# Kernel optimization log

Measured on AMD Instinct MI355X. Metric: run time of the kernel, lower is better.

## Reference

```python
import jax, jax.numpy as jnp
import numpy as np

N = 50000          # nodes
E = 1_600_000      # edges (before self-loops)
F_IN = 256
HID = 32
HEADS = 4
OUT = 64
NEG_SLOPE = 0.2


def setup_inputs() -> dict:
    key = jax.random.key(0)
    ks = jax.random.split(key, 10)
    x = jax.random.normal(ks[0], (N, F_IN), dtype=jnp.float32)
    edge_index = jax.random.randint(ks[1], (2, E), 0, N, dtype=jnp.int64)
    # layer 1: input_dim -> hidden*heads
    W1 = jax.random.normal(ks[2], (F_IN, HEADS * HID), dtype=jnp.float32) / np.sqrt(F_IN)
    att_src1 = jax.random.normal(ks[3], (HEADS, HID), dtype=jnp.float32) / np.sqrt(HID)
    att_dst1 = jax.random.normal(ks[4], (HEADS, HID), dtype=jnp.float32) / np.sqrt(HID)
    b1 = jnp.zeros((HEADS * HID,), dtype=jnp.float32)
    # layer 2: hidden*heads -> out, 1 head, concat=False
    W2 = jax.random.normal(ks[5], (HEADS * HID, OUT), dtype=jnp.float32) / np.sqrt(HEADS * HID)
    att_src2 = jax.random.normal(ks[6], (1, OUT), dtype=jnp.float32) / np.sqrt(OUT)
    att_dst2 = jax.random.normal(ks[7], (1, OUT), dtype=jnp.float32) / np.sqrt(OUT)
    b2 = jnp.zeros((OUT,), dtype=jnp.float32)
    return {"x": x, "edge_index": edge_index, "W1": W1, "att_src1": att_src1,
            "att_dst1": att_dst1, "b1": b1, "W2": W2, "att_src2": att_src2,
            "att_dst2": att_dst2, "b2": b2}


def gat_layer(x, src, dst, W, a_src, a_dst, bias, heads, out_dim, concat):
    n = x.shape[0]
    h = (x @ W).reshape(n, heads, out_dim)              # [N,H,C]
    # per-node attention logits
    al_src = jnp.sum(h * a_src[None], axis=-1)          # [N,H]
    al_dst = jnp.sum(h * a_dst[None], axis=-1)          # [N,H]
    e = al_src[src] + al_dst[dst]                       # [E',H]
    e = jax.nn.leaky_relu(e, NEG_SLOPE)
    # segment softmax over incoming edges of each dst node
    emax = jax.ops.segment_max(e, dst, num_segments=n)  # [N,H]
    ee = jnp.exp(e - emax[dst])
    denom = jax.ops.segment_sum(ee, dst, num_segments=n)
    alpha = ee / denom[dst]                             # [E',H]
    msg = h[src] * alpha[:, :, None]                    # [E',H,C]
    out = jax.ops.segment_sum(msg, dst, num_segments=n)  # [N,H,C]
    if concat:
        out = out.reshape(n, heads * out_dim)
    else:
        out = out.mean(axis=1)
    return out + bias


def reference(x, edge_index, W1, att_src1, att_dst1, b1, W2, att_src2, att_dst2, b2):
    # add self-loops (PyG GATConv default)
    loop = jnp.arange(N, dtype=edge_index.dtype)
    src = jnp.concatenate([edge_index[0], loop])
    dst = jnp.concatenate([edge_index[1], loop])
    # eval mode: dropout(p=0.5) is identity
    h = gat_layer(x, src, dst, W1, att_src1, att_dst1, b1, HEADS, HID, True)
    h = jax.nn.elu(h)
    out = gat_layer(h, src, dst, W2, att_src2, att_dst2, b2, 1, OUT, False)
    return out
```

## Files before the change

kernel.cpp:

```cpp
#include <hip/hip_runtime.h>
#include <hip/hip_bf16.h>
#include <hip/hip_fp16.h>
#include <math.h>

#define NNODES 50000
#define NEDGES 1600000
#define ETOT   (NEDGES + NNODES)
#define F_INN  256
#define NEG_SLOPE 0.2f
#define NBUCK  782
#define BCAP   2624
#define CNBLK  256
#define CBT    1024

__global__ __launch_bounds__(128) void detect_kernel(const unsigned int* __restrict__ ei,
                                                     int* __restrict__ flag) {
    __shared__ int nz;
    if (threadIdx.x == 0) nz = 0;
    __syncthreads();
    unsigned int v = ei[2 * threadIdx.x + 1];
    if (v != 0u) nz = 1;
    __syncthreads();
    if (threadIdx.x == 0) *flag = nz;
}

__device__ __forceinline__ void load_edge(const void* ei, bool is32, int i, int& s, int& d) {
    if (i < NEDGES) {
        if (is32) {
            const int* p = (const int*)ei;
            s = p[i]; d = p[NEDGES + i];
        } else {
            const long long* p = (const long long*)ei;
            s = (int)p[i]; d = (int)p[NEDGES + i];
        }
    } else {
        s = i - NEDGES; d = s;
    }
}

__global__ __launch_bounds__(CBT) void convert_kernel(const void* __restrict__ ei,
                                                      const int* __restrict__ flag,
                                                      int* __restrict__ bcnt,
                                                      int2* __restrict__ bpair) {
    __shared__ int hist[NBUCK];
    __shared__ int base[NBUCK];
    const int t = threadIdx.x;
    const int chunk = (ETOT + CNBLK - 1) / CNBLK;
    const int i0 = blockIdx.x * chunk;
    const int i1 = min(i0 + chunk, ETOT);
    for (int k = t; k < NBUCK; k += CBT) hist[k] = 0;
    __syncthreads();
    const bool is32 = (*flag) != 0;
    for (int i = i0 + t; i < i1; i += CBT) {
        int s, d; load_edge(ei, is32, i, s, d);
        atomicAdd(&hist[d >> 6], 1);
    }
    __syncthreads();
    for (int k = t; k < NBUCK; k += CBT) {
        int c = hist[k];
        base[k] = c ? atomicAdd(&bcnt[k], c) : 0;
        hist[k] = 0;
    }
    __syncthreads();
    for (int i = i0 + t; i < i1; i += CBT) {
        int s, d; load_edge(ei, is32, i, s, d);
        int b = d >> 6;
        int pos = base[b] + atomicAdd(&hist[b], 1);
        bpair[(size_t)b * BCAP + pos] = make_int2(s, d);
    }
}

__global__ __launch_bounds__(1024) void bucket_scan_kernel(const int* __restrict__ bcnt,
                                                           int* __restrict__ bbase,
                                                           int* __restrict__ rowptr) {
    __shared__ int wsum[16];
    const int t = threadIdx.x, lane = t & 63, wid = t >> 6;
    int v = (t < NBUCK) ? bcnt[t] : 0;
    int incl = v;
    #pragma unroll
    for (int off = 1; off < 64; off <<= 1) {
        int u = __shfl_up(incl, off);
        if (lane >= off) incl += u;
    }
    if (lane == 63) wsum[wid] = incl;
    __syncthreads();
    if (wid == 0) {
        int wv = (lane < 16) ? wsum[lane] : 0;
        #pragma unroll
        for (int off = 1; off < 16; off <<= 1) {
            int u = __shfl_up(wv, off);
            if (lane >= off) wv += u;
        }
        if (lane < 16) wsum[lane] = wv;
    }
    __syncthreads();
    int base = (wid == 0) ? 0 : wsum[wid - 1];
    if (t < NBUCK) bbase[t] = base + incl - v;
    if (t == 0) rowptr[NNODES] = ETOT;
}

__global__ __launch_bounds__(256) void bscatter_kernel(const int2* __restrict__ bpair,
                                                       const int* __restrict__ bcnt,
                                                       const int* __restrict__ bbase,
                                                       int* __restrict__ rowptr,
                                                       int* __restrict__ ssrc) {
    __shared__ int cnt[64];
    __shared__ int s_widx[64];
    const int b = blockIdx.x;
    const int t = threadIdx.x;
    if (t < 64) cnt[t] = 0;
    __syncthreads();
    const int n = bcnt[b];
    const int2* bp = bpair + (size_t)b * BCAP;
    for (int i = t; i < n; i += 256) atomicAdd(&cnt[bp[i].y & 63], 1);
    __syncthreads();
    if (t < 64) {
        int v = cnt[t];
        int incl = v;
        #pragma unroll
        for (int off = 1; off < 64; off <<= 1) {
            int u = __shfl_up(incl, off);
            if (t >= off) incl += u;
        }
        int excl = bbase[b] + incl - v;
        int node = (b << 6) + t;
        if (node < NNODES) rowptr[node] = excl;
        s_widx[t] = excl;
    }
    __syncthreads();
    for (int i = t; i < n; i += 256) {
        int2 e = bp[i];
        int pos = atomicAdd(&s_widx[e.y & 63], 1);
        ssrc[pos] = e.x;
    }
}

__global__ __launch_bounds__(256) void gemm1_kernel(const float* __restrict__ x,
                                                    const float* __restrict__ W,
                                                    const float* __restrict__ atts,
                                                    const float* __restrict__ attd,
                                                    __half2* __restrict__ h1h,
                                                    float* __restrict__ als,
                                                    float* __restrict__ ald) {
    __shared__ float xs[32][68];
    __shared__ float ws[32][128];
    const int tid = threadIdx.x;
    const int tx = tid & 15, ty = tid >> 4;
    const int row0 = blockIdx.x * 64;
    float acc[4][8];
    #pragma unroll
    for (int r = 0; r < 4; ++r)
        #pragma unroll
        for (int c = 0; c < 8; ++c) acc[r][c] = 0.f;

    const int lr = tid >> 2;
    const int lk = (tid & 3) * 8;
    const int wk = tid >> 3;
    const int wc = (tid & 7) * 16;

    for (int k0 = 0; k0 < F_INN; k0 += 32) {
        float4 v0 = make_float4(0.f,0.f,0.f,0.f), v1 = v0;
        int gr = row0 + lr;
        if (gr < NNODES) {
            const float* xp = x + (size_t)gr * F_INN + k0 + lk;
            v0 = *(const float4*)xp; v1 = *(const float4*)(xp + 4);
        }
        xs[lk+0][lr]=v0.x; xs[lk+1][lr]=v0.y; xs[lk+2][lr]=v0.z; xs[lk+3][lr]=v0.w;
        xs[lk+4][lr]=v1.x; xs[lk+5][lr]=v1.y; xs[lk+6][lr]=v1.z; xs[lk+7][lr]=v1.w;
        const float* wp = W + (size_t)(k0 + wk) * 128 + wc;
        #pragma unroll
        for (int q = 0; q < 4; ++q)
            *(float4*)&ws[wk][wc + q*4] = *(const float4*)(wp + q*4);
        __syncthreads();
        #pragma unroll
        for (int k = 0; k < 32; ++k) {
            float4 av = *(const float4*)&xs[k][ty*4];
            float4 b0 = *(const float4*)&ws[k][tx*8];
            float4 b1 = *(const float4*)&ws[k][tx*8+4];
            const float a_[4] = {av.x,av.y,av.z,av.w};
            const float b_[8] = {b0.x,b0.y,b0.z,b0.w,b1.x,b1.y,b1.z,b1.w};
            #pragma unroll
            for (int r = 0; r < 4; ++r)
                #pragma unroll
                for (int c = 0; c < 8; ++c)
                    acc[r][c] = fmaf(a_[r], b_[c], acc[r][c]);
        }
        __syncthreads();
    }
    #pragma unroll
    for (int r = 0; r < 4; ++r) {
        int gr = row0 + ty*4 + r;
        bool valid = gr < NNODES;
        float ps = 0.f, pd = 0.f;
        if (valid) {
            float4 pack;
            __half2* pk = (__half2*)&pack;
            pk[0] = __floats2half2_rn(acc[r][0], acc[r][1]);
            pk[1] = __floats2half2_rn(acc[r][2], acc[r][3]);
            pk[2] = __floats2half2_rn(acc[r][4], acc[r][5]);
            pk[3] = __floats2half2_rn(acc[r][6], acc[r][7]);
            *(float4*)(h1h + (size_t)gr*64 + tx*4) = pack;
            #pragma unroll
            for (int c = 0; c < 8; ++c) {
                ps = fmaf(acc[r][c], atts[tx*8 + c], ps);
                pd = fmaf(acc[r][c], attd[tx*8 + c], pd);
            }
        }
        ps += __shfl_xor(ps, 1); ps += __shfl_xor(ps, 2);
        pd += __shfl_xor(pd, 1); pd += __shfl_xor(pd, 2);
        if (valid && (tx & 3) == 0) {
            int hd = tx >> 2;
            als[gr*4 + hd] = ps;
            ald[gr*4 + hd] = pd;
        }
    }
}

__global__ __launch_bounds__(256) void gemm2_kernel(const float* __restrict__ x2,
                                                    const float* __restrict__ W,
                                                    const float* __restrict__ atts,
                                                    const float* __restrict__ attd,
                                                    float* __restrict__ h2,
                                                    float* __restrict__ als,
                                                    float* __restrict__ ald) {
    __shared__ float xs[32][68];
    __shared__ float ws[32][64];
    const int tid = threadIdx.x;
    const int tx = tid & 15, ty = tid >> 4;
    const int row0 = blockIdx.x * 64;
    float acc[4][4];
    #pragma unroll
    for (int r = 0; r < 4; ++r)
        #pragma unroll
        for (int c = 0; c < 4; ++c) acc[r][c] = 0.f;

    const int lr = tid >> 2;
    const int lk = (tid & 3) * 8;
    const int wk = tid >> 3;
    const int wc = (tid & 7) * 8;

    for (int k0 = 0; k0 < 128; k0 += 32) {
        float4 v0 = make_float4(0.f,0.f,0.f,0.f), v1 = v0;
        int gr = row0 + lr;
        if (gr < NNODES) {
            const float* xp = x2 + (size_t)gr * 128 + k0 + lk;
            v0 = *(const float4*)xp; v1 = *(const float4*)(xp + 4);
        }
        xs[lk+0][lr]=v0.x; xs[lk+1][lr]=v0.y; xs[lk+2][lr]=v0.z; xs[lk+3][lr]=v0.w;
        xs[lk+4][lr]=v1.x; xs[lk+5][lr]=v1.y; xs[lk+6][lr]=v1.z; xs[lk+7][lr]=v1.w;
        const float* wp = W + (size_t)(k0 + wk) * 64 + wc;
        *(float4*)&ws[wk][wc]     = *(const float4*)wp;
        *(float4*)&ws[wk][wc + 4] = *(const float4*)(wp + 4);
        __syncthreads();
        #pragma unroll
        for (int k = 0; k < 32; ++k) {
            float4 av = *(const float4*)&xs[k][ty*4];
            float4 bv = *(const float4*)&ws[k][tx*4];
            const float a_[4] = {av.x,av.y,av.z,av.w};
            const float b_[4] = {bv.x,bv.y,bv.z,bv.w};
            #pragma unroll
            for (int r = 0; r < 4; ++r)
                #pragma unroll
                for (int c = 0; c < 4; ++c)
                    acc[r][c] = fmaf(a_[r], b_[c], acc[r][c]);
        }
        __syncthreads();
    }
    #pragma unroll
    for (int r = 0; r < 4; ++r) {
        int gr = row0 + ty*4 + r;
        bool valid = gr < NNODES;
        float ps = 0.f, pd = 0.f;
        if (valid) {
            *(float4*)&h2[(size_t)gr*64 + tx*4] = make_float4(acc[r][0],acc[r][1],acc[r][2],acc[r][3]);
            #pragma unroll
            for (int c = 0; c < 4; ++c) {
                ps = fmaf(acc[r][c], atts[tx*4 + c], ps);
                pd = fmaf(acc[r][c], attd[tx*4 + c], pd);
            }
        }
        ps += __shfl_xor(ps, 1); ps += __shfl_xor(ps, 2);
        ps += __shfl_xor(ps, 4); ps += __shfl_xor(ps, 8);
        pd += __shfl_xor(pd, 1); pd += __shfl_xor(pd, 2);
        pd += __shfl_xor(pd, 4); pd += __shfl_xor(pd, 8);
        if (valid && tx == 0) {
            als[gr] = ps;
            ald[gr] = pd;
        }
    }
}

__device__ __forceinline__ float lrelu(float e) { return e > 0.f ? e : NEG_SLOPE * e; }

__global__ __launch_bounds__(256) void edge1_kernel(const int* __restrict__ rowptr,
                                                    const int* __restrict__ ssrc,
                                                    const float* __restrict__ als,
                                                    const float* __restrict__ ald,
                                                    const __half2* __restrict__ h1h,
                                                    const float* __restrict__ b1,
                                                    float* __restrict__ x2) {
    __shared__ float s_alpha[4][256];
    __shared__ int   s_sidx[4][64];
    __shared__ int   s_nch[4];
    const int lane = threadIdx.x & 63;
    const int wid  = threadIdx.x >> 6;
    const int d = blockIdx.x * 4 + wid;
    const int start = rowptr[d], end = rowptr[d + 1];
    const int deg = end - start;
    float4 aldv = *(const float4*)&ald[d * 4];

    float l0=0.f, l1=0.f, l2=0.f, l3=0.f;
    float4 ex0 = make_float4(0,0,0,0), ex1 = ex0;
    int ss0 = 0, ss1 = 0;
    int it = 0;
    for (int j = start + lane; j < end; j += 64, ++it) {
        int s = ssrc[j];
        float4 a = *(const float4*)&als[s * 4];
        float e0 = __expf(lrelu(a.x + aldv.x));
        float e1 = __expf(lrelu(a.y + aldv.y));
        float e2 = __expf(lrelu(a.z + aldv.z));
        float e3 = __expf(lrelu(a.w + aldv.w));
        if (it == 0)      { ex0 = make_float4(e0,e1,e2,e3); ss0 = s; }
        else if (it == 1) { ex1 = make_float4(e0,e1,e2,e3); ss1 = s; }
        l0 += e0; l1 += e1; l2 += e2; l3 += e3;
    }
    #pragma unroll
    for (int off = 32; off >= 1; off >>= 1) {
        l0 += __shfl_xor(l0, off); l1 += __shfl_xor(l1, off);
        l2 += __shfl_xor(l2, off); l3 += __shfl_xor(l3, off);
    }
    float il0 = 1.f/l0, il1 = 1.f/l1, il2 = 1.f/l2, il3 = 1.f/l3;

    const int nch = (deg + 63) >> 6;
    if (lane == 0) s_nch[wid] = nch;
    __syncthreads();
    const int maxch = max(max(s_nch[0], s_nch[1]), max(s_nch[2], s_nch[3]));

    const int h = lane >> 4;
    float s0 = 0.f, s1 = 0.f;
    for (int c = 0; c < maxch; ++c) {
        const int base = start + c * 64;
        if (c < nch) {
            int j = base + lane;
            if (j < end) {
                int s; float4 ex;
                if (c == 0)      { s = ss0; ex = ex0; }
                else if (c == 1) { s = ss1; ex = ex1; }
                else {
                    s = ssrc[j];
                    float4 a = *(const float4*)&als[s * 4];
                    ex = make_float4(__expf(lrelu(a.x + aldv.x)),
                                     __expf(lrelu(a.y + aldv.y)),
                                     __expf(lrelu(a.z + aldv.z)),
                                     __expf(lrelu(a.w + aldv.w)));
                }
                s_sidx[wid][lane] = s;
                float4 al = make_float4(ex.x*il0, ex.y*il1, ex.z*il2, ex.w*il3);
                *(float4*)&s_alpha[wid][lane * 4] = al;
            }
        }
        __syncthreads();
        if (c < nch) {
            const int cnt = min(64, end - base);
            int jj = 0;
            for (; jj + 3 < cnt; jj += 4) {
                int sA = __builtin_amdgcn_readfirstlane(s_sidx[wid][jj]);
                int sB = __builtin_amdgcn_readfirstlane(s_sidx[wid][jj + 1]);
                int sC = __builtin_amdgcn_readfirstlane(s_sidx[wid][jj + 2]);
                int sD = __builtin_amdgcn_readfirstlane(s_sidx[wid][jj + 3]);
                float aA = s_alpha[wid][jj*4 + h];
                float aB = s_alpha[wid][jj*4 + 4 + h];
                float aC = s_alpha[wid][jj*4 + 8 + h];
                float aD = s_alpha[wid][jj*4 + 12 + h];
                float2 hA = __half22float2(h1h[(size_t)sA * 64 + lane]);
                float2 hB = __half22float2(h1h[(size_t)sB * 64 + lane]);
                float2 hC = __half22float2(h1h[(size_t)sC * 64 + lane]);
                float2 hD = __half22float2(h1h[(size_t)sD * 64 + lane]);
                s0 = fmaf(hA.x, aA, s0); s1 = fmaf(hA.y, aA, s1);
                s0 = fmaf(hB.x, aB, s0); s1 = fmaf(hB.y, aB, s1);
                s0 = fmaf(hC.x, aC, s0); s1 = fmaf(hC.y, aC, s1);
                s0 = fmaf(hD.x, aD, s0); s1 = fmaf(hD.y, aD, s1);
            }
            for (; jj < cnt; ++jj) {
                int sA = __builtin_amdgcn_readfirstlane(s_sidx[wid][jj]);
                float aA = s_alpha[wid][jj*4 + h];
                float2 hA = __half22float2(h1h[(size_t)sA * 64 + lane]);
                s0 = fmaf(hA.x, aA, s0); s1 = fmaf(hA.y, aA, s1);
            }
        }
        __syncthreads();
    }
    const int col = lane << 1;
    float o0 = s0 + b1[col], o1 = s1 + b1[col + 1];
    o0 = o0 > 0.f ? o0 : expm1f(o0);
    o1 = o1 > 0.f ? o1 : expm1f(o1);
    *(float2*)&x2[(size_t)d * 128 + col] = make_float2(o0, o1);
}

__global__ __launch_bounds__(256) void edge2_kernel(const int* __restrict__ rowptr,
                                                    const int* __restrict__ ssrc,
                                                    const float* __restrict__ als,
                                                    const float* __restrict__ ald,
                                                    const float* __restrict__ h2,
                                                    const float* __restrict__ b2,
                                                    float* __restrict__ out) {
    __shared__ float s_alpha[4][64];
    __shared__ int   s_sidx[4][64];
    __shared__ int   s_nch[4];
    const int lane = threadIdx.x & 63;
    const int wid  = threadIdx.x >> 6;
    const int d = blockIdx.x * 4 + wid;
    const int start = rowptr[d], end = rowptr[d + 1];
    const int deg = end - start;
    float aldd = ald[d];

    float l = 0.f;
    float ex0 = 0.f, ex1 = 0.f;
    int ss0 = 0, ss1 = 0;
    int it = 0;
    for (int j = start + lane; j < end; j += 64, ++it) {
        int s = ssrc[j];
        float e = __expf(lrelu(als[s] + aldd));
        if (it == 0)      { ex0 = e; ss0 = s; }
        else if (it == 1) { ex1 = e; ss1 = s; }
        l += e;
    }
    #pragma unroll
    for (int off = 32; off >= 1; off >>= 1) l += __shfl_xor(l, off);
    float invl = 1.f / l;

    const int nch = (deg + 63) >> 6;
    if (lane == 0) s_nch[wid] = nch;
    __syncthreads();
    const int maxch = max(max(s_nch[0], s_nch[1]), max(s_nch[2], s_nch[3]));

    float acc = 0.f;
    for (int c = 0; c < maxch; ++c) {
        const int base = start + c * 64;
        if (c < nch) {
            int j = base + lane;
            if (j < end) {
                int s; float e;
                if (c == 0)      { s = ss0; e = ex0; }
                else if (c == 1) { s = ss1; e = ex1; }
                else { s = ssrc[j]; e = __expf(lrelu(als[s] + aldd)); }
                s_sidx[wid][lane] = s;
                s_alpha[wid][lane] = e * invl;
            }
        }
        __syncthreads();
        if (c < nch) {
            const int cnt = min(64, end - base);
            int jj = 0;
            for (; jj + 3 < cnt; jj += 4) {
                int sA = __builtin_amdgcn_readfirstlane(s_sidx[wid][jj]);
                int sB = __builtin_amdgcn_readfirstlane(s_sidx[wid][jj + 1]);
                int sC = __builtin_amdgcn_readfirstlane(s_sidx[wid][jj + 2]);
                int sD = __builtin_amdgcn_readfirstlane(s_sidx[wid][jj + 3]);
                float aA = s_alpha[wid][jj],     aB = s_alpha[wid][jj + 1];
                float aC = s_alpha[wid][jj + 2], aD = s_alpha[wid][jj + 3];
                float hA = h2[(size_t)sA * 64 + lane];
                float hB = h2[(size_t)sB * 64 + lane];
                float hC = h2[(size_t)sC * 64 + lane];
                float hD = h2[(size_t)sD * 64 + lane];
                acc = fmaf(hA, aA, acc);
                acc = fmaf(hB, aB, acc);
                acc = fmaf(hC, aC, acc);
                acc = fmaf(hD, aD, acc);
            }
            for (; jj < cnt; ++jj) {
                int sA = __builtin_amdgcn_readfirstlane(s_sidx[wid][jj]);
                float aA = s_alpha[wid][jj];
                acc = fmaf(h2[(size_t)sA * 64 + lane], aA, acc);
            }
        }
        __syncthreads();
    }
    out[(size_t)d * 64 + lane] = acc + b2[lane];
}

extern "C" void kernel_launch(void* const* d_in, const int* in_sizes, int n_in,
                              void* d_out, int out_size, void* d_ws, size_t ws_size,
                              hipStream_t stream) {
    const float* x   = (const float*)d_in[0];
    const void*  ei  = d_in[1];
    const float* W1  = (const float*)d_in[2];
    const float* as1 = (const float*)d_in[3];
    const float* ad1 = (const float*)d_in[4];
    const float* b1  = (const float*)d_in[5];
    const float* W2  = (const float*)d_in[6];
    const float* as2 = (const float*)d_in[7];
    const float* ad2 = (const float*)d_in[8];
    const float* b2  = (const float*)d_in[9];
    float* out = (float*)d_out;

    char* p = (char*)d_ws;
    auto alloc = [&](size_t bytes) {
        char* r = p;
        p += (bytes + 255) & ~(size_t)255;
        return r;
    };
    int2*     bpair  = (int2*)alloc(sizeof(int2) * (size_t)NBUCK * BCAP);
    int*      bcnt   = (int*)alloc(sizeof(int) * NBUCK);
    int*      bbase  = (int*)alloc(sizeof(int) * NBUCK);
    int*      ssrc   = (int*)alloc(sizeof(int) * ETOT);
    int*      rowptr = (int*)alloc(sizeof(int) * (NNODES + 1));
    int*      flag   = (int*)alloc(256);
    float*    als1   = (float*)alloc(sizeof(float) * NNODES * 4);
    float*    ald1   = (float*)alloc(sizeof(float) * NNODES * 4);
    float*    als2v  = (float*)alloc(sizeof(float) * NNODES);
    float*    ald2v  = (float*)alloc(sizeof(float) * NNODES);
    __half2*  h1h    = (__half2*)alloc(sizeof(__half2) * NNODES * 64);
    float*    x2     = (float*)alloc(sizeof(float) * NNODES * 128);
    float*    h2     = (float*)alloc(sizeof(float) * NNODES * 64);

    hipMemsetAsync(bcnt, 0, sizeof(int) * NBUCK, stream);

    detect_kernel<<<1, 128, 0, stream>>>((const unsigned int*)ei, flag);
    convert_kernel<<<CNBLK, CBT, 0, stream>>>(ei, flag, bcnt, bpair);
    bucket_scan_kernel<<<1, 1024, 0, stream>>>(bcnt, bbase, rowptr);
    bscatter_kernel<<<NBUCK, 256, 0, stream>>>(bpair, bcnt, bbase, rowptr, ssrc);
    gemm1_kernel<<<(NNODES + 63) / 64, 256, 0, stream>>>(x, W1, as1, ad1, h1h, als1, ald1);
    edge1_kernel<<<(NNODES + 3) / 4, 256, 0, stream>>>(rowptr, ssrc, als1, ald1, h1h, b1, x2);
    gemm2_kernel<<<(NNODES + 63) / 64, 256, 0, stream>>>(x2, W2, as2, ad2, h2, als2v, ald2v);
    edge2_kernel<<<(NNODES + 3) / 4, 256, 0, stream>>>(rowptr, ssrc, als2v, ald2v, h2, b2, out);
}
```

Measured before the change: 343.6 us.

## Double-buffer shared tiles with register prefetch and XOR swizzle in both GEMMs

Both projection GEMMs now prefetch the next K-slice of x and W into registers while computing on the current shared-memory buffer, then store it into a second buffer. This leaves one barrier per iteration instead of two and overlaps global load latency with FMAs. The transposed x tile also uses an XOR swizzle on the column index to reduce LDS bank conflicts on the scattered stores, and the W tile gets padding. The cost is double the shared memory per block and more live registers, which may lower occupancy.

```diff
diff --git a/kernel.cpp b/kernel.cpp
--- a/kernel.cpp
+++ b/kernel.cpp
@@ -142,8 +142,8 @@
                                                     __half2* __restrict__ h1h,
                                                     float* __restrict__ als,
                                                     float* __restrict__ ald) {
-    __shared__ float xs[32][68];
-    __shared__ float ws[32][128];
+    __shared__ float xs[2][32][68];
+    __shared__ float ws[2][32][132];
     const int tid = threadIdx.x;
     const int tx = tid & 15, ty = tid >> 4;
     const int row0 = blockIdx.x * 64;
@@ -155,28 +155,47 @@
 
     const int lr = tid >> 2;
     const int lk = (tid & 3) * 8;
+    const int sw = (lk & 8) << 1;
+    const int cl = lr ^ sw;
     const int wk = tid >> 3;
     const int wc = (tid & 7) * 16;
 
-    for (int k0 = 0; k0 < F_INN; k0 += 32) {
-        float4 v0 = make_float4(0.f,0.f,0.f,0.f), v1 = v0;
-        int gr = row0 + lr;
-        if (gr < NNODES) {
-            const float* xp = x + (size_t)gr * F_INN + k0 + lk;
-            v0 = *(const float4*)xp; v1 = *(const float4*)(xp + 4);
-        }
-        xs[lk+0][lr]=v0.x; xs[lk+1][lr]=v0.y; xs[lk+2][lr]=v0.z; xs[lk+3][lr]=v0.w;
-        xs[lk+4][lr]=v1.x; xs[lk+5][lr]=v1.y; xs[lk+6][lr]=v1.z; xs[lk+7][lr]=v1.w;
-        const float* wp = W + (size_t)(k0 + wk) * 128 + wc;
-        #pragma unroll
-        for (int q = 0; q < 4; ++q)
-            *(float4*)&ws[wk][wc + q*4] = *(const float4*)(wp + q*4);
-        __syncthreads();
+    const int gr = row0 + lr;
+    const bool gok = gr < NNODES;
+    const float* xpb = x + (size_t)gr * F_INN + lk;
+    const float* wpb = W + (size_t)wk * 128 + wc;
+
+    float4 rx0 = make_float4(0,0,0,0), rx1 = rx0;
+    float4 rw0, rw1, rw2, rw3;
+    if (gok) { rx0 = *(const float4*)xpb; rx1 = *(const float4*)(xpb + 4); }
+    rw0 = *(const float4*)(wpb);      rw1 = *(const float4*)(wpb + 4);
+    rw2 = *(const float4*)(wpb + 8);  rw3 = *(const float4*)(wpb + 12);
+    xs[0][lk+0][cl]=rx0.x; xs[0][lk+1][cl]=rx0.y; xs[0][lk+2][cl]=rx0.z; xs[0][lk+3][cl]=rx0.w;
+    xs[0][lk+4][cl]=rx1.x; xs[0][lk+5][cl]=rx1.y; xs[0][lk+6][cl]=rx1.z; xs[0][lk+7][cl]=rx1.w;
+    *(float4*)&ws[0][wk][wc]      = rw0;
+    *(float4*)&ws[0][wk][wc + 4]  = rw1;
+    *(float4*)&ws[0][wk][wc + 8]  = rw2;
+    *(float4*)&ws[0][wk][wc + 12] = rw3;
+    __syncthreads();
+
+    for (int k0 = 0; k0 < 8; ++k0) {
+        const int cur = k0 & 1;
+        const bool more = (k0 < 7);
+        if (more) {
+            const int kk = (k0 + 1) * 32;
+            if (gok) {
+                const float* xp = xpb + kk;
+                rx0 = *(const float4*)xp; rx1 = *(const float4*)(xp + 4);
+            }
+            const float* wp = wpb + (size_t)kk * 128;
+            rw0 = *(const float4*)(wp);      rw1 = *(const float4*)(wp + 4);
+            rw2 = *(const float4*)(wp + 8);  rw3 = *(const float4*)(wp + 12);
+        }
         #pragma unroll
         for (int k = 0; k < 32; ++k) {
-            float4 av = *(const float4*)&xs[k][ty*4];
-            float4 b0 = *(const float4*)&ws[k][tx*8];
-            float4 b1 = *(const float4*)&ws[k][tx*8+4];
+            float4 av = *(const float4*)&xs[cur][k][(ty*4) ^ ((k & 8) << 1)];
+            float4 b0 = *(const float4*)&ws[cur][k][tx*8];
+            float4 b1 = *(const float4*)&ws[cur][k][tx*8+4];
             const float a_[4] = {av.x,av.y,av.z,av.w};
             const float b_[8] = {b0.x,b0.y,b0.z,b0.w,b1.x,b1.y,b1.z,b1.w};
             #pragma unroll
@@ -185,12 +204,22 @@
                 for (int c = 0; c < 8; ++c)
                     acc[r][c] = fmaf(a_[r], b_[c], acc[r][c]);
         }
+        if (more) {
+            const int nb = cur ^ 1;
+            xs[nb][lk+0][cl]=rx0.x; xs[nb][lk+1][cl]=rx0.y; xs[nb][lk+2][cl]=rx0.z; xs[nb][lk+3][cl]=rx0.w;
+            xs[nb][lk+4][cl]=rx1.x; xs[nb][lk+5][cl]=rx1.y; xs[nb][lk+6][cl]=rx1.z; xs[nb][lk+7][cl]=rx1.w;
+            *(float4*)&ws[nb][wk][wc]      = rw0;
+            *(float4*)&ws[nb][wk][wc + 4]  = rw1;
+            *(float4*)&ws[nb][wk][wc + 8]  = rw2;
+            *(float4*)&ws[nb][wk][wc + 12] = rw3;
+        }
         __syncthreads();
     }
+
     #pragma unroll
     for (int r = 0; r < 4; ++r) {
-        int gr = row0 + ty*4 + r;
-        bool valid = gr < NNODES;
+        int gor = row0 + ty*4 + r;
+        bool valid = gor < NNODES;
         float ps = 0.f, pd = 0.f;
         if (valid) {
             float4 pack;
@@ -199,7 +228,7 @@
             pk[1] = __floats2half2_rn(acc[r][2], acc[r][3]);
             pk[2] = __floats2half2_rn(acc[r][4], acc[r][5]);
             pk[3] = __floats2half2_rn(acc[r][6], acc[r][7]);
-            *(float4*)(h1h + (size_t)gr*64 + tx*4) = pack;
+            *(float4*)(h1h + (size_t)gor*64 + tx*4) = pack;
             #pragma unroll
             for (int c = 0; c < 8; ++c) {
                 ps = fmaf(acc[r][c], atts[tx*8 + c], ps);
@@ -210,8 +239,8 @@
         pd += __shfl_xor(pd, 1); pd += __shfl_xor(pd, 2);
         if (valid && (tx & 3) == 0) {
             int hd = tx >> 2;
-            als[gr*4 + hd] = ps;
-            ald[gr*4 + hd] = pd;
+            als[gor*4 + hd] = ps;
+            ald[gor*4 + hd] = pd;
         }
     }
 }
@@ -223,8 +252,8 @@
                                                     float* __restrict__ h2,
                                                     float* __restrict__ als,
                                                     float* __restrict__ ald) {
-    __shared__ float xs[32][68];
-    __shared__ float ws[32][64];
+    __shared__ float xs[2][32][68];
+    __shared__ float ws[2][32][68];
     const int tid = threadIdx.x;
     const int tx = tid & 15, ty = tid >> 4;
     const int row0 = blockIdx.x * 64;
@@ -236,26 +265,42 @@
 
     const int lr = tid >> 2;
     const int lk = (tid & 3) * 8;
+    const int sw = (lk & 8) << 1;
+    const int cl = lr ^ sw;
     const int wk = tid >> 3;
     const int wc = (tid & 7) * 8;
 
-    for (int k0 = 0; k0 < 128; k0 += 32) {
-        float4 v0 = make_float4(0.f,0.f,0.f,0.f), v1 = v0;
-        int gr = row0 + lr;
-        if (gr < NNODES) {
-            const float* xp = x2 + (size_t)gr * 128 + k0 + lk;
-            v0 = *(const float4*)xp; v1 = *(const float4*)(xp + 4);
-        }
-        xs[lk+0][lr]=v0.x; xs[lk+1][lr]=v0.y; xs[lk+2][lr]=v0.z; xs[lk+3][lr]=v0.w;
-        xs[lk+4][lr]=v1.x; xs[lk+5][lr]=v1.y; xs[lk+6][lr]=v1.z; xs[lk+7][lr]=v1.w;
-        const float* wp = W + (size_t)(k0 + wk) * 64 + wc;
-        *(float4*)&ws[wk][wc]     = *(const float4*)wp;
-        *(float4*)&ws[wk][wc + 4] = *(const float4*)(wp + 4);
-        __syncthreads();
+    const int gr = row0 + lr;
+    const bool gok = gr < NNODES;
+    const float* xpb = x2 + (size_t)gr * 128 + lk;
+    const float* wpb = W + (size_t)wk * 64 + wc;
+
+    float4 rx0 = make_float4(0,0,0,0), rx1 = rx0;
+    float4 rw0, rw1;
+    if (gok) { rx0 = *(const float4*)xpb; rx1 = *(const float4*)(xpb + 4); }
+    rw0 = *(const float4*)(wpb); rw1 = *(const float4*)(wpb + 4);
+    xs[0][lk+0][cl]=rx0.x; xs[0][lk+1][cl]=rx0.y; xs[0][lk+2][cl]=rx0.z; xs[0][lk+3][cl]=rx0.w;
+    xs[0][lk+4][cl]=rx1.x; xs[0][lk+5][cl]=rx1.y; xs[0][lk+6][cl]=rx1.z; xs[0][lk+7][cl]=rx1.w;
+    *(float4*)&ws[0][wk][wc]     = rw0;
+    *(float4*)&ws[0][wk][wc + 4] = rw1;
+    __syncthreads();
+
+    for (int k0 = 0; k0 < 4; ++k0) {
+        const int cur = k0 & 1;
+        const bool more = (k0 < 3);
+        if (more) {
+            const int kk = (k0 + 1) * 32;
+            if (gok) {
+                const float* xp = xpb + kk;
+                rx0 = *(const float4*)xp; rx1 = *(const float4*)(xp + 4);
+            }
+            const float* wp = wpb + (size_t)kk * 64;
+            rw0 = *(const float4*)(wp); rw1 = *(const float4*)(wp + 4);
+        }
         #pragma unroll
         for (int k = 0; k < 32; ++k) {
-            float4 av = *(const float4*)&xs[k][ty*4];
-            float4 bv = *(const float4*)&ws[k][tx*4];
+            float4 av = *(const float4*)&xs[cur][k][(ty*4) ^ ((k & 8) << 1)];
+            float4 bv = *(const float4*)&ws[cur][k][tx*4];
             const float a_[4] = {av.x,av.y,av.z,av.w};
             const float b_[4] = {bv.x,bv.y,bv.z,bv.w};
             #pragma unroll
@@ -264,15 +309,23 @@
                 for (int c = 0; c < 4; ++c)
                     acc[r][c] = fmaf(a_[r], b_[c], acc[r][c]);
         }
+        if (more) {
+            const int nb = cur ^ 1;
+            xs[nb][lk+0][cl]=rx0.x; xs[nb][lk+1][cl]=rx0.y; xs[nb][lk+2][cl]=rx0.z; xs[nb][lk+3][cl]=rx0.w;
+            xs[nb][lk+4][cl]=rx1.x; xs[nb][lk+5][cl]=rx1.y; xs[nb][lk+6][cl]=rx1.z; xs[nb][lk+7][cl]=rx1.w;
+            *(float4*)&ws[nb][wk][wc]     = rw0;
+            *(float4*)&ws[nb][wk][wc + 4] = rw1;
+        }
         __syncthreads();
     }
+
     #pragma unroll
     for (int r = 0; r < 4; ++r) {
-        int gr = row0 + ty*4 + r;
-        bool valid = gr < NNODES;
+        int gor = row0 + ty*4 + r;
+        bool valid = gor < NNODES;
         float ps = 0.f, pd = 0.f;
         if (valid) {
-            *(float4*)&h2[(size_t)gr*64 + tx*4] = make_float4(acc[r][0],acc[r][1],acc[r][2],acc[r][3]);
+            *(float4*)&h2[(size_t)gor*64 + tx*4] = make_float4(acc[r][0],acc[r][1],acc[r][2],acc[r][3]);
             #pragma unroll
             for (int c = 0; c < 4; ++c) {
                 ps = fmaf(acc[r][c], atts[tx*4 + c], ps);
@@ -284,8 +337,8 @@
         pd += __shfl_xor(pd, 1); pd += __shfl_xor(pd, 2);
         pd += __shfl_xor(pd, 4); pd += __shfl_xor(pd, 8);
         if (valid && tx == 0) {
-            als[gr] = ps;
-            ald[gr] = pd;
+            als[gor] = ps;
+            ald[gor] = pd;
         }
     }
 }
```

Result: slower. 389.6 us (+13.4%).
